# Kernel optimization log

Measured on AMD Instinct MI355X. Metric: run time of the kernel, lower is better.

Reference implementation:

```python
import jax, jax.numpy as jnp
import numpy as np
jax.config.update("jax_enable_x64", True)

T_OLD = 60000
T_NEW = 60000
NV = 30000
MAX_STEPS = 300
FB_CHUNK = 500  # T_OLD must be divisible by this

FACE_OPP = np.array([[1, 2, 3], [0, 2, 3], [0, 1, 3], [0, 1, 2]])
EDGES = [(0, 1), (0, 2), (0, 3), (1, 2), (1, 3), (2, 3)]


def setup_inputs() -> dict:
    key = jax.random.key(0)
    k1, k2, k3, k4, k5 = jax.random.split(key, 5)
    # distinct vertices per tet (sorted base + strictly increasing offsets)
    off = jnp.arange(4, dtype=jnp.int64)
    new_indices = jnp.sort(jax.random.randint(k1, (T_NEW, 4), 0, NV - 4, dtype=jnp.int64), axis=1) + off
    old_indices = jnp.sort(jax.random.randint(k2, (T_OLD, 4), 0, NV - 4, dtype=jnp.int64), axis=1) + off
    return {
        "new_indices": new_indices,
        "old_indices": old_indices,
        "old_cc": jax.random.normal(k3, (T_OLD, 3), dtype=jnp.float32),
        "new_cc": jax.random.normal(k4, (T_NEW, 3), dtype=jnp.float32),
        "vertex_positions": jax.random.uniform(k5, (NV, 3), dtype=jnp.float32),
    }


def _min_edge_length(verts, indices):
    p = verts[indices]  # (T,4,3)
    el = jnp.stack([jnp.linalg.norm(p[:, a] - p[:, b], axis=-1) for a, b in EDGES])
    return el.min(axis=0)


def _forward(new_indices, old_indices, old_cc, new_cc, vertex_positions):
    T_new = new_indices.shape[0]
    T_old = old_indices.shape[0]
    Vn = vertex_positions.shape[0]

    # --- 1. unchanged-tet detection via sorted-vertex int64 keys ---
    key4 = lambda s: ((s[:, 0] * Vn + s[:, 1]) * Vn + s[:, 2]) * Vn + s[:, 3]
    ok = key4(jnp.sort(old_indices, axis=1))
    nk = key4(jnp.sort(new_indices, axis=1))
    order = jnp.argsort(ok)
    sk = ok[order]
    pos = jnp.searchsorted(sk, nk, side='right') - 1
    posc = jnp.clip(pos, 0, T_old - 1)
    matched = jnp.where((pos >= 0) & (sk[posc] == nk), order[posc], -1)
    is_matched = matched >= 0
    matched_safe = jnp.maximum(matched, 0)

    # --- 2. face adjacency of old mesh (sorted face keys, adjacent-equal pairing) ---
    fi = jnp.sort(old_indices[:, FACE_OPP], axis=2)          # (T_old,4,3)
    fk = (fi[..., 0] * Vn + fi[..., 1]) * Vn + fi[..., 2]    # (T_old,4)
    all_keys = fk.T.reshape(-1)                              # f-major like the numpy concat
    all_tets = jnp.tile(jnp.arange(T_old), 4)
    all_locals = jnp.repeat(jnp.arange(4), T_old)
    o2 = jnp.argsort(all_keys)
    sk2, st, sl = all_keys[o2], all_tets[o2], all_locals[o2]
    same = sk2[:-1] == sk2[1:]
    neighbors = jnp.full((T_old, 4), -1, dtype=jnp.int64)
    neighbors = neighbors.at[jnp.where(same, st[:-1], T_old), sl[:-1]].set(st[1:], mode='drop')
    neighbors = neighbors.at[jnp.where(same, st[1:], T_old), sl[1:]].set(st[:-1], mode='drop')

    # --- 3. per-old-tet inverse edge matrix; degenerate tets get no neighbors ---
    verts = jax.lax.stop_gradient(vertex_positions).astype(jnp.float32)
    p = verts[old_indices]                                   # (T_old,4,3)
    v0 = p[:, 0]
    Tm = jnp.stack([p[:, 1] - v0, p[:, 2] - v0, p[:, 3] - v0], axis=-1)
    degen = jnp.abs(jnp.linalg.det(Tm)) < 1e-10
    Tinv = jnp.linalg.inv(jnp.where(degen[:, None, None], jnp.eye(3, dtype=Tm.dtype), Tm))
    neighbors = jnp.where(degen[:, None], -1, neighbors)

    prio = jnp.full((Vn,), -1, dtype=jnp.int64)
    ar = jnp.arange(T_old)
    for vi in range(4):
        prio = prio.at[old_indices[:, vi]].max(vi * T_old + ar)
    v2t = jnp.where(prio >= 0, prio % T_old, 0)

    # --- 5. barycentric walk (masked, all float inputs stop-gradiented; int outputs) ---
    cent = jax.lax.stop_gradient(verts[new_indices].mean(axis=1))  # (T_new,3)
    seed = v2t[new_indices[:, 0]]
    n_walk = jnp.sum(~is_matched)
    thr = jnp.maximum(jnp.int64(100), n_walk // 1000)

    def cond(state):
        step, cur, rem, act = state
        return (step < MAX_STEPS) & (jnp.sum(act) >= thr)

    def body(state):
        step, cur, rem, act = state
        rel = cent - v0[cur]
        bary = jnp.einsum('nij,nj->ni', Tinv[cur], rel)
        all_b = jnp.concatenate([(1.0 - bary.sum(axis=1))[:, None], bary], axis=1)
        conv = act & (all_b.min(axis=1) >= -1e-4)
        rem = jnp.where(conv, cur, rem)
        act = act & ~conv
        nb = neighbors[cur, jnp.argmin(all_b, axis=1)]
        at_bd = act & (nb < 0)
        rem = jnp.where(at_bd, cur, rem)
        act = act & ~at_bd
        cur = jnp.where(act, nb, cur)
        return (step + 1, cur, rem, act)

    _, cur, rem, act = jax.lax.while_loop(cond, body, (jnp.int64(0), seed, seed, ~is_matched))
    rem = jnp.where(act, cur, rem)

    # --- 6. nearest-centroid fallback for unfinished walks (gated, chunked) ---
    old_cents = jax.lax.stop_gradient(verts[old_indices].mean(axis=1))

    def fallback(_):
        p2 = (cent ** 2).sum(-1)
        c2 = (old_cents ** 2).sum(-1)
        def scan_body(carry, i):
            bd, bi = carry
            c = jax.lax.dynamic_slice(old_cents, (i * FB_CHUNK, 0), (FB_CHUNK, 3))
            cn = jax.lax.dynamic_slice(c2, (i * FB_CHUNK,), (FB_CHUNK,))
            d = p2[:, None] - 2.0 * (cent @ c.T) + cn[None, :]
            md = d.min(axis=1)
            mi = d.argmin(axis=1).astype(jnp.int64) + i * FB_CHUNK
            imp = md < bd
            return (jnp.where(imp, md, bd), jnp.where(imp, mi, bi)), None
        init = (jnp.full((T_new,), jnp.inf, dtype=jnp.float32), jnp.zeros((T_new,), dtype=jnp.int64))
        (bd, bi), _ = jax.lax.scan(scan_body, init, jnp.arange(T_old // FB_CHUNK))
        return bi

    fb = jax.lax.cond(jnp.sum(act) > 0, fallback, lambda _: jnp.zeros((T_new,), dtype=jnp.int64), None)
    rem = jnp.clip(jnp.where(act, fb, rem), 0, T_old - 1)
    remap = jnp.where(is_matched, matched_safe, rem)

    # --- 7. candidates: containing tet + 4 face neighbors ---
    face_nb = neighbors[remap]
    face_nb = jnp.where(face_nb >= 0, face_nb, remap[:, None])
    cands = jnp.concatenate([remap[:, None], face_nb], axis=1)            # (T_new,5)
    cands = jnp.where(is_matched[:, None], matched_safe[:, None], cands)

    # --- 8. overlap / circumcenter-distance weights ---
    cand_verts = old_indices[cands]                                       # (T_new,5,4)
    overlap = (cand_verts[:, :, :, None] == new_indices[:, None, None, :]).any(-1).sum(-1).astype(jnp.float32)
    cc_d2 = ((old_cc[cands] - new_cc[:, None, :]) ** 2).sum(-1)
    raw = jnp.exp(overlap * 2.0) / (cc_d2 + 1e-8)
    weights = raw / raw.sum(axis=1, keepdims=True)

    # --- 9. density scale: min-edge-length ratio ---
    old_el = _min_edge_length(vertex_positions, old_indices)[cands]
    new_el = _min_edge_length(vertex_positions, new_indices)
    density_scale = jnp.clip(old_el / jnp.maximum(new_el[:, None], 1e-8), 0.1, 10.0)

    return cands, weights, density_scale


_forward_jit = jax.jit(_forward)


def reference(new_indices, old_indices, old_cc, new_cc, vertex_positions):
    return _forward_jit(new_indices, old_indices, old_cc, new_cc, vertex_positions)
```

## Files before the change

### kernel.cpp

```cpp
#include <hip/hip_runtime.h>

#pragma clang fp contract(off)

#define TOLD 60000
#define TNEW 60000
#define NVERT 30000
#define MAXSTEPS 300
#define THSZ 131072
#define FHSZ 131072
#define EMPTY64 0xFFFFFFFFFFFFFFFFULL
#define NWGR 60
#define VRANGE 500
#define NSLICE 16
#define TSLICE (TOLD / NSLICE)

#define NB_SETUP 235
#define NB_PRIO  (NWGR * NSLICE)
#define NB_NEWG  235
#define NB_FACE  938
#define NB_FOLD  118
#define NB_MATCH 235
#define NB_FB    120
#define FBRANGE  (TNEW / NB_FB)

#define OFF_TKEYS    0u
#define OFF_FTAB     1048576u
#define OFF_NBR      2097152u
#define FF_BYTES     3057152u
#define OFF_CNT      3057152u
#define OFF_TVALS    3059200u
#define OFF_PPRIO    3583488u
#define OFF_PRIO     5503488u
#define OFF_IDXOLD   5623488u
#define OFF_SSTEP    6583488u
#define OFF_DEGEN    6823488u
#define OFF_MATCHED  7063488u
#define OFF_TV4      7303488u
#define OFF_COLD4    10183488u
#define OFF_CNEW4    11143488u
#define OFF_DM       12103488u

struct P {
  const unsigned int* rawNew;
  const unsigned int* rawOld;
  const float* occ;
  const float* ncc;
  const float* verts;
  float* out;
  unsigned long long* tkeys;
  unsigned long long* ftab;
  int* counters;
  int* tvals;
  int* idxOld;
  int* nbr;
  int* pprio;
  int* prio;
  int* sstep;
  int* degen;
  int* matched;
  float4* Tv4;
  float4* cold4;
  float4* cnew4;
  unsigned long long* dm;
  unsigned int dmMask;
};

__device__ __forceinline__ unsigned hash64(unsigned long long k){
  k ^= k >> 33; k *= 0xff51afd7ed558ccdULL;
  k ^= k >> 33; k *= 0xc4ceb9fe1a85ec53ULL;
  k ^= k >> 33;
  return (unsigned)k;
}
__device__ __forceinline__ void cswap(int& a, int& b){ if (a > b){ int t = a; a = b; b = t; } }

__device__ __forceinline__ int detect64(const unsigned int* raw){
  unsigned acc = 0;
  const uint4* r4 = (const uint4*)raw;
  #pragma unroll
  for (int k = 0; k < 32; ++k){ uint4 v = r4[k]; acc |= (v.y | v.w); }
  return acc == 0u;
}

__device__ __forceinline__ int4 load_tet4(const unsigned int* raw, int is64, int t){
  if (is64){
    uint4 a = ((const uint4*)raw)[t * 2 + 0];
    uint4 b = ((const uint4*)raw)[t * 2 + 1];
    return make_int4((int)a.x, (int)a.z, (int)b.x, (int)b.z);
  }
  uint4 a = ((const uint4*)raw)[t];
  return make_int4((int)a.x, (int)a.y, (int)a.z, (int)a.w);
}

__device__ __forceinline__ void face_insert(unsigned long long* ftab, int* nbr,
                                            unsigned long long fkey, int t, int l){
  unsigned long long mine = (fkey << 18) | (unsigned long long)(t * 4 + l);
  unsigned slot = hash64(fkey ^ 0x9e3779b97f4a7c15ULL) & (FHSZ - 1);
  while (true){
    unsigned long long prev = atomicCAS(&ftab[slot], EMPTY64, mine);
    if (prev == EMPTY64) return;
    if ((prev >> 18) == fkey){
      int oid = (int)(prev & 0x3FFFFULL);
      nbr[t * 4 + l] = oid >> 2;
      nbr[oid] = t;
      return;
    }
    slot = (slot + 1) & (FHSZ - 1);
  }
}

__device__ __forceinline__ float min_edge_r(
    float q0x, float q0y, float q0z, float q1x, float q1y, float q1z,
    float q2x, float q2y, float q2z, float q3x, float q3y, float q3z){
  float m = 3.402823466e+38f;
  float dx, dy, dz, d;
  dx = q0x - q1x; dy = q0y - q1y; dz = q0z - q1z; d = sqrtf((dx*dx + dy*dy) + dz*dz); m = fminf(m, d);
  dx = q0x - q2x; dy = q0y - q2y; dz = q0z - q2z; d = sqrtf((dx*dx + dy*dy) + dz*dz); m = fminf(m, d);
  dx = q0x - q3x; dy = q0y - q3y; dz = q0z - q3z; d = sqrtf((dx*dx + dy*dy) + dz*dz); m = fminf(m, d);
  dx = q1x - q2x; dy = q1y - q2y; dz = q1z - q2z; d = sqrtf((dx*dx + dy*dy) + dz*dz); m = fminf(m, d);
  dx = q1x - q3x; dy = q1y - q3y; dz = q1z - q3z; d = sqrtf((dx*dx + dy*dy) + dz*dz); m = fminf(m, d);
  dx = q2x - q3x; dy = q2y - q3y; dz = q2z - q3z; d = sqrtf((dx*dx + dy*dy) + dz*dz); m = fminf(m, d);
  return m;
}

__global__ __launch_bounds__(256) void k_front(P p){
  __shared__ int sprio[VRANGE];
  int bb = blockIdx.x;
  if (bb < NB_SETUP){
    int t = bb * 256 + threadIdx.x;
    if (bb == 0){
      for (int j = threadIdx.x; j < 384; j += 256) p.counters[j] = 0;
    }
    if (t >= TOLD) return;
    int is64 = detect64(p.rawOld);
    int4 iv4 = load_tet4(p.rawOld, is64, t);
    int i0 = iv4.x, i1 = iv4.y, i2 = iv4.z, i3 = iv4.w;
    ((int4*)p.idxOld)[t] = iv4;

    {
      int s0 = i0, s1 = i1, s2 = i2, s3 = i3;
      cswap(s0, s1); cswap(s2, s3); cswap(s0, s2); cswap(s1, s3); cswap(s1, s2);
      unsigned long long key =
          (unsigned long long)((((long long)s0 * NVERT + s1) * NVERT + s2) * NVERT + s3);
      unsigned slot = hash64(key) & (THSZ - 1);
      while (true){
        unsigned long long prev = atomicCAS(&p.tkeys[slot], EMPTY64, key);
        if (prev == EMPTY64){ p.tvals[slot] = t; break; }
        if (prev == key){ atomicMax(&p.tvals[slot], t); break; }
        slot = (slot + 1) & (THSZ - 1);
      }
    }

    if (p.dmMask){
      const int FO[4][3] = {{1, 2, 3}, {0, 2, 3}, {0, 1, 3}, {0, 1, 2}};
      int iv[4] = {i0, i1, i2, i3};
      #pragma unroll
      for (int l = 0; l < 4; ++l){
        int a = iv[FO[l][0]], b = iv[FO[l][1]], c = iv[FO[l][2]];
        cswap(a, b); cswap(a, c); cswap(b, c);
        unsigned long long fk = (unsigned long long)(((long long)a * NVERT + b) * NVERT + c);
        p.dm[hash64(fk) & p.dmMask] = (fk << 18) | (unsigned long long)(t * 4 + l);
      }
    }

    float q0x = p.verts[i0 * 3 + 0], q0y = p.verts[i0 * 3 + 1], q0z = p.verts[i0 * 3 + 2];
    float q1x = p.verts[i1 * 3 + 0], q1y = p.verts[i1 * 3 + 1], q1z = p.verts[i1 * 3 + 2];
    float q2x = p.verts[i2 * 3 + 0], q2y = p.verts[i2 * 3 + 1], q2z = p.verts[i2 * 3 + 2];
    float q3x = p.verts[i3 * 3 + 0], q3y = p.verts[i3 * 3 + 1], q3z = p.verts[i3 * 3 + 2];
    float e1x = q1x - q0x, e1y = q1y - q0y, e1z = q1z - q0z;
    float e2x = q2x - q0x, e2y = q2y - q0y, e2z = q2z - q0z;
    float e3x = q3x - q0x, e3y = q3y - q0y, e3z = q3z - q0z;
    float c23x = e2y * e3z - e2z * e3y;
    float c23y = e2z * e3x - e2x * e3z;
    float c23z = e2x * e3y - e2y * e3x;
    float det = e1x * c23x + e1y * c23y + e1z * c23z;
    int dg = (fabsf(det) < 1e-10f) ? 1 : 0;
    p.degen[t] = dg;
    float4 r0, r1, r2;
    if (dg){
      r0 = make_float4(1.f, 0.f, 0.f, q0x);
      r1 = make_float4(0.f, 1.f, 0.f, q0y);
      r2 = make_float4(0.f, 0.f, 1.f, q0z);
    } else {
      float inv = 1.0f / det;
      float c31x = e3y * e1z - e3z * e1y;
      float c31y = e3z * e1x - e3x * e1z;
      float c31z = e3x * e1y - e3y * e1x;
      float c12x = e1y * e2z - e1z * e2y;
      float c12y = e1z * e2x - e1x * e2z;
      float c12z = e1x * e2y - e1y * e2x;
      r0 = make_float4(c23x * inv, c23y * inv, c23z * inv, q0x);
      r1 = make_float4(c31x * inv, c31y * inv, c31z * inv, q0y);
      r2 = make_float4(c12x * inv, c12y * inv, c12z * inv, q0z);
    }
    p.Tv4[t * 3 + 0] = r0;
    p.Tv4[t * 3 + 1] = r1;
    p.Tv4[t * 3 + 2] = r2;
    float el = min_edge_r(q0x, q0y, q0z, q1x, q1y, q1z, q2x, q2y, q2z, q3x, q3y, q3z);
    p.cold4[t] = make_float4((((q0x + q1x) + q2x) + q3x) * 0.25f,
                             (((q0y + q1y) + q2y) + q3y) * 0.25f,
                             (((q0z + q1z) + q2z) + q3z) * 0.25f, el);
  } else if (bb < NB_SETUP + NB_PRIO){
    int rb = bb - NB_SETUP;
    int range = rb / NSLICE;
    int slice = rb % NSLICE;
    int base = range * VRANGE;
    for (int j = threadIdx.x; j < VRANGE; j += 256) sprio[j] = -1;
    __syncthreads();
    int is64 = detect64(p.rawOld);
    int t0 = slice * TSLICE;
    for (int t = t0 + threadIdx.x; t < t0 + TSLICE; t += 256){
      int4 iv = load_tet4(p.rawOld, is64, t);
      int v;
      v = iv.x - base; if ((unsigned)v < VRANGE) atomicMax(&sprio[v], 0 * TOLD + t);
      v = iv.y - base; if ((unsigned)v < VRANGE) atomicMax(&sprio[v], 1 * TOLD + t);
      v = iv.z - base; if ((unsigned)v < VRANGE) atomicMax(&sprio[v], 2 * TOLD + t);
      v = iv.w - base; if ((unsigned)v < VRANGE) atomicMax(&sprio[v], 3 * TOLD + t);
    }
    __syncthreads();
    for (int j = threadIdx.x; j < VRANGE; j += 256)
      p.pprio[slice * NVERT + base + j] = sprio[j];
  } else {
    int n = (bb - NB_SETUP - NB_PRIO) * 256 + threadIdx.x;
    if (n >= TNEW) return;
    int is64 = detect64(p.rawNew);
    int4 ni = load_tet4(p.rawNew, is64, n);
    float q0x = p.verts[ni.x * 3 + 0], q0y = p.verts[ni.x * 3 + 1], q0z = p.verts[ni.x * 3 + 2];
    float q1x = p.verts[ni.y * 3 + 0], q1y = p.verts[ni.y * 3 + 1], q1z = p.verts[ni.y * 3 + 2];
    float q2x = p.verts[ni.z * 3 + 0], q2y = p.verts[ni.z * 3 + 1], q2z = p.verts[ni.z * 3 + 2];
    float q3x = p.verts[ni.w * 3 + 0], q3y = p.verts[ni.w * 3 + 1], q3z = p.verts[ni.w * 3 + 2];
    float el = min_edge_r(q0x, q0y, q0z, q1x, q1y, q1z, q2x, q2y, q2z, q3x, q3y, q3z);
    p.cnew4[n] = make_float4((((q0x + q1x) + q2x) + q3x) * 0.25f,
                             (((q0y + q1y) + q2y) + q3y) * 0.25f,
                             (((q0z + q1z) + q2z) + q3z) * 0.25f, el);
  }
}

__global__ __launch_bounds__(256) void k_mid(P p){
  int bb = blockIdx.x;
  if (bb < NB_FACE){
    int i = bb * 256 + threadIdx.x;
    if (i >= TOLD * 4) return;
    int t = i >> 2, l = i & 3;
    int4 iv4 = ((const int4*)p.idxOld)[t];
    int iv[4] = {iv4.x, iv4.y, iv4.z, iv4.w};
    const int FO[4][3] = {{1, 2, 3}, {0, 2, 3}, {0, 1, 3}, {0, 1, 2}};
    int a = iv[FO[l][0]], b = iv[FO[l][1]], c = iv[FO[l][2]];
    cswap(a, b); cswap(a, c); cswap(b, c);
    unsigned long long fk = (unsigned long long)(((long long)a * NVERT + b) * NVERT + c);
    if (p.dmMask){
      unsigned long long mine = (fk << 18) | (unsigned long long)i;
      unsigned long long got = p.dm[hash64(fk) & p.dmMask];
      if (got == mine) return;
      if ((got >> 18) == fk){
        int wid = (int)(got & 0x3FFFFULL);
        p.nbr[i] = wid >> 2;
        p.nbr[wid] = t;
        return;
      }
    }
    face_insert(p.ftab, p.nbr, fk, t, l);
  } else if (bb < NB_FACE + NB_FOLD){
    int v = (bb - NB_FACE) * 256 + threadIdx.x;
    if (v >= NVERT) return;
    int pr = -1;
    #pragma unroll
    for (int s = 0; s < NSLICE; ++s) pr = max(pr, p.pprio[s * NVERT + v]);
    p.prio[v] = pr;
  } else {
    int n = (bb - NB_FACE - NB_FOLD) * 256 + threadIdx.x;
    if (n >= TNEW) return;
    int is64 = detect64(p.rawNew);
    int4 ni = load_tet4(p.rawNew, is64, n);
    int s0 = ni.x, s1 = ni.y, s2 = ni.z, s3 = ni.w;
    cswap(s0, s1); cswap(s2, s3); cswap(s0, s2); cswap(s1, s3); cswap(s1, s2);
    unsigned long long key =
        (unsigned long long)((((long long)s0 * NVERT + s1) * NVERT + s2) * NVERT + s3);
    int m = -1;
    unsigned slot = hash64(key) & (THSZ - 1);
    while (true){
      unsigned long long k = p.tkeys[slot];
      if (k == EMPTY64) break;
      if (k == key){ m = p.tvals[slot]; break; }
      slot = (slot + 1) & (THSZ - 1);
    }
    p.matched[n] = m;
  }
}

__device__ __forceinline__ void assemble_walker(const P& p, int n, int m, int remap){
  int cds[5];
  if (m >= 0){
    cds[0] = cds[1] = cds[2] = cds[3] = cds[4] = m;
  } else {
    cds[0] = remap;
    int dg = p.degen[remap];
    int4 nb4 = ((const int4*)p.nbr)[remap];
    int nbl[4] = {nb4.x, nb4.y, nb4.z, nb4.w};
    for (int l = 0; l < 4; ++l){
      int fb = dg ? -1 : nbl[l];
      cds[1 + l] = (fb >= 0) ? fb : remap;
    }
  }
  bool same = (cds[1] == cds[0]) & (cds[2] == cds[0]) &
              (cds[3] == cds[0]) & (cds[4] == cds[0]);
  int is64 = detect64(p.rawNew);
  int4 ni = load_tet4(p.rawNew, is64, n);
  float nc0 = p.ncc[n * 3 + 0], nc1 = p.ncc[n * 3 + 1], nc2 = p.ncc[n * 3 + 2];
  float nelv = fmaxf(p.cnew4[n].w, 1e-8f);
  if (same){
    int ct = cds[0];
    int4 cv = ((const int4*)p.idxOld)[ct];
    int ov = 0;
    ov += (cv.x == ni.x || cv.x == ni.y || cv.x == ni.z || cv.x == ni.w) ? 1 : 0;
    ov += (cv.y == ni.x || cv.y == ni.y || cv.y == ni.z || cv.y == ni.w) ? 1 : 0;
    ov += (cv.z == ni.x || cv.z == ni.y || cv.z == ni.z || cv.z == ni.w) ? 1 : 0;
    ov += (cv.w == ni.x || cv.w == ni.y || cv.w == ni.z || cv.w == ni.w) ? 1 : 0;
    float d0 = p.occ[ct * 3 + 0] - nc0;
    float d1 = p.occ[ct * 3 + 1] - nc1;
    float d2 = p.occ[ct * 3 + 2] - nc2;
    float ccd2 = (d0 * d0 + d1 * d1) + d2 * d2;
    float raw = expf((float)ov * 2.0f) / (ccd2 + 1e-8f);
    float rsum = 0.0f;
    rsum += raw; rsum += raw; rsum += raw; rsum += raw; rsum += raw;
    float wgt = raw / rsum;
    float ds = p.cold4[ct].w / nelv;
    ds = fminf(fmaxf(ds, 0.1f), 10.0f);
    float cf = (float)ct;
    for (int c = 0; c < 5; ++c){
      p.out[n * 5 + c] = cf;
      p.out[TNEW * 5 + n * 5 + c] = wgt;
      p.out[2 * TNEW * 5 + n * 5 + c] = ds;
    }
    return;
  }
  float raws[5]; float rsum = 0.0f;
  float oels[5];
  for (int c = 0; c < 5; ++c){
    int ct = cds[c];
    int4 cv = ((const int4*)p.idxOld)[ct];
    int ov = 0;
    ov += (cv.x == ni.x || cv.x == ni.y || cv.x == ni.z || cv.x == ni.w) ? 1 : 0;
    ov += (cv.y == ni.x || cv.y == ni.y || cv.y == ni.z || cv.y == ni.w) ? 1 : 0;
    ov += (cv.z == ni.x || cv.z == ni.y || cv.z == ni.z || cv.z == ni.w) ? 1 : 0;
    ov += (cv.w == ni.x || cv.w == ni.y || cv.w == ni.z || cv.w == ni.w) ? 1 : 0;
    float d0 = p.occ[ct * 3 + 0] - nc0;
    float d1 = p.occ[ct * 3 + 1] - nc1;
    float d2 = p.occ[ct * 3 + 2] - nc2;
    float ccd2 = (d0 * d0 + d1 * d1) + d2 * d2;
    float raw = expf((float)ov * 2.0f) / (ccd2 + 1e-8f);
    raws[c] = raw; rsum += raw;
    oels[c] = p.cold4[ct].w;
  }
  for (int c = 0; c < 5; ++c){
    p.out[n * 5 + c] = (float)cds[c];
    p.out[TNEW * 5 + n * 5 + c] = raws[c] / rsum;
    float ds = oels[c] / nelv;
    ds = fminf(fmaxf(ds, 0.1f), 10.0f);
    p.out[2 * TNEW * 5 + n * 5 + c] = ds;
  }
}

__global__ __launch_bounds__(256) void k_walkall(P p){
  __shared__ int s_hist[MAXSTEPS + 2];
  __shared__ int s_nw;
  for (int j = threadIdx.x; j < MAXSTEPS + 2; j += 256) s_hist[j] = 0;
  if (threadIdx.x == 0) s_nw = 0;
  __syncthreads();
  int n = blockIdx.x * blockDim.x + threadIdx.x;
  if (n < TNEW){
    int m = p.matched[n];
    if (m >= 0){
      assemble_walker(p, n, m, 0);
    } else {
      atomicAdd(&s_nw, 1);
      int is64 = detect64(p.rawNew);
      int i0 = is64 ? (int)((const long long*)p.rawNew)[n * 4] : ((const int*)p.rawNew)[n * 4];
      int pr = p.prio[i0];
      int c = (pr >= 0) ? (pr % TOLD) : 0;
      float4 cn = p.cnew4[n];
      int s = MAXSTEPS + 1;
      for (int k = 1; k <= MAXSTEPS; ++k){
        float4 r0 = p.Tv4[c * 3 + 0];
        float4 r1 = p.Tv4[c * 3 + 1];
        float4 r2 = p.Tv4[c * 3 + 2];
        float rx = cn.x - r0.w, ry = cn.y - r1.w, rz = cn.z - r2.w;
        float b0 = r0.x * rx + r0.y * ry + r0.z * rz;
        float b1 = r1.x * rx + r1.y * ry + r1.z * rz;
        float b2 = r2.x * rx + r2.y * ry + r2.z * rz;
        float a0 = 1.0f - (b0 + b1 + b2);
        float ab[4] = {a0, b0, b1, b2};
        int amin = 0; float mn = ab[0];
        for (int j = 1; j < 4; ++j){ if (ab[j] < mn){ mn = ab[j]; amin = j; } }
        if (mn >= -0.0001f){ s = k; break; }
        int nb = p.degen[c] ? -1 : p.nbr[c * 4 + amin];
        if (nb < 0){ s = k; break; }
        c = nb;
      }
      p.sstep[n] = s;
      atomicAdd(&s_hist[s], 1);
      assemble_walker(p, n, -1, c);
    }
  }
  __syncthreads();
  if (threadIdx.x == 0 && s_nw) atomicAdd(&p.counters[0], s_nw);
  for (int j = threadIdx.x; j < MAXSTEPS + 2; j += 256){
    int v = s_hist[j];
    if (v) atomicAdd(&p.counters[64 + j], v);
  }
}

__device__ __forceinline__ int compute_S(const int* counters){
  int nw = counters[0];
  int thr = max(100, nw / 1000);
  if (nw < thr) return 0;
  int cnt = nw;
  for (int k = 1; k <= MAXSTEPS; ++k){
    cnt -= counters[64 + k];
    if (cnt < thr) return k;
  }
  return MAXSTEPS;
}

__global__ __launch_bounds__(256) void k_tail(P p){
  __shared__ float sd[256];
  __shared__ int si[256];
  __shared__ int s_hits[256];
  __shared__ int s_nhits;
  __shared__ int s_S;
  if (threadIdx.x == 0) s_S = compute_S(p.counters);
  __syncthreads();
  int S = s_S;
  int base = blockIdx.x * FBRANGE;
  for (int chunk = base; chunk < base + FBRANGE; chunk += 256){
    if (threadIdx.x == 0) s_nhits = 0;
    __syncthreads();
    int n = chunk + threadIdx.x;
    if (n < base + FBRANGE && n < TNEW){
      if (p.matched[n] < 0 && p.sstep[n] > S)
        s_hits[atomicAdd(&s_nhits, 1)] = n;
    }
    __syncthreads();
    int nh = s_nhits;
    for (int h = 0; h < nh; ++h){
      int n2 = s_hits[h];
      float4 cn = p.cnew4[n2];
      float cx = cn.x, cy = cn.y, cz = cn.z;
      float p2 = (cx * cx + cy * cy) + cz * cz;
      float bd = 3.402823466e+38f; int bi = 0;
      for (int j = threadIdx.x; j < TOLD; j += 256){
        float4 oc = p.cold4[j];
        float dot = (cx * oc.x + cy * oc.y) + cz * oc.z;
        float c2 = (oc.x * oc.x + oc.y * oc.y) + oc.z * oc.z;
        float d = (p2 - 2.0f * dot) + c2;
        if (d < bd || (d == bd && j < bi)){ bd = d; bi = j; }
      }
      sd[threadIdx.x] = bd; si[threadIdx.x] = bi;
      __syncthreads();
      for (int s = 128; s > 0; s >>= 1){
        if ((int)threadIdx.x < s){
          float od = sd[threadIdx.x + s]; int oi = si[threadIdx.x + s];
          if (od < sd[threadIdx.x] || (od == sd[threadIdx.x] && oi < si[threadIdx.x])){
            sd[threadIdx.x] = od; si[threadIdx.x] = oi;
          }
        }
        __syncthreads();
      }
      if (threadIdx.x == 0){
        int r = si[0];
        if (r < 0) r = 0; if (r > TOLD - 1) r = TOLD - 1;
        assemble_walker(p, n2, -1, r);
      }
      __syncthreads();
    }
    __syncthreads();
  }
}

extern "C" void kernel_launch(void* const* d_in, const int* in_sizes, int n_in,
                              void* d_out, int out_size, void* d_ws, size_t ws_size,
                              hipStream_t stream) {
  char* w = (char*)d_ws;
  P p;
  p.rawNew = (const unsigned int*)d_in[0];
  p.rawOld = (const unsigned int*)d_in[1];
  p.occ    = (const float*)d_in[2];
  p.ncc    = (const float*)d_in[3];
  p.verts  = (const float*)d_in[4];
  p.out    = (float*)d_out;
  p.tkeys    = (unsigned long long*)(w + OFF_TKEYS);
  p.ftab     = (unsigned long long*)(w + OFF_FTAB);
  p.nbr      = (int*)(w + OFF_NBR);
  p.counters = (int*)(w + OFF_CNT);
  p.tvals    = (int*)(w + OFF_TVALS);
  p.pprio    = (int*)(w + OFF_PPRIO);
  p.prio     = (int*)(w + OFF_PRIO);
  p.idxOld   = (int*)(w + OFF_IDXOLD);
  p.sstep    = (int*)(w + OFF_SSTEP);
  p.degen    = (int*)(w + OFF_DEGEN);
  p.matched  = (int*)(w + OFF_MATCHED);
  p.Tv4      = (float4*)(w + OFF_TV4);
  p.cold4    = (float4*)(w + OFF_COLD4);
  p.cnew4    = (float4*)(w + OFF_CNEW4);
  p.dm       = (unsigned long long*)(w + OFF_DM);
  size_t avail = (ws_size > (size_t)OFF_DM) ? ws_size - (size_t)OFF_DM : 0;
  unsigned dmMask = 0;
  for (int bshift = 21; bshift >= 16; --bshift){
    if (avail >= ((size_t)8 << bshift)){ dmMask = (1u << bshift) - 1u; break; }
  }
  p.dmMask = dmMask;

  hipMemsetAsync(w, 0xFF, FF_BYTES, stream);
  hipLaunchKernelGGL(k_front,   dim3(NB_SETUP + NB_PRIO + NB_NEWG), dim3(256), 0, stream, p);
  hipLaunchKernelGGL(k_mid,     dim3(NB_FACE + NB_FOLD + NB_MATCH), dim3(256), 0, stream, p);
  hipLaunchKernelGGL(k_walkall, dim3((TNEW + 255) / 256), dim3(256), 0, stream, p);
  hipLaunchKernelGGL(k_tail,    dim3(NB_FB), dim3(256), 0, stream, p);
}
```

Before: 113.7 us.

## Replace CAS tet hash with direct-mapped table plus fallback, fuse match into walker

Tet-key deduplication now writes keys into a large direct-mapped table without atomics. Duplicate resolution and collisions are deferred to the face pass, where a CAS-based fallback table handles them. The workspace memset is replaced by init blocks inside the first kernel, and new-tet geometry and the match lookup move into the walker kernel, removing the separate matched array and an extra pass. Correctness depends on the non-atomic direct-map writes: the key write for a slot can race, and setting tval2 by plain store loses last-write-wins semantics when duplicate keys exist.

Result: faster. 109.5 us (-3.7%).

```diff
diff --git a/kernel.cpp b/kernel.cpp
--- a/kernel.cpp
+++ b/kernel.cpp
@@ -6,7 +6,8 @@
 #define TNEW 60000
 #define NVERT 30000
 #define MAXSTEPS 300
-#define THSZ 131072
+#define TKSZ 262144
+#define TFBSZ 131072
 #define FHSZ 131072
 #define EMPTY64 0xFFFFFFFFFFFFFFFFULL
 #define NWGR 60
@@ -16,29 +17,31 @@
 
 #define NB_SETUP 235
 #define NB_PRIO  (NWGR * NSLICE)
-#define NB_NEWG  235
+#define NB_INIT  187
 #define NB_FACE  938
 #define NB_FOLD  118
-#define NB_MATCH 235
+#define NB_WALK  235
 #define NB_FB    120
 #define FBRANGE  (TNEW / NB_FB)
 
-#define OFF_TKEYS    0u
-#define OFF_FTAB     1048576u
+#define OFF_FTAB     0u
+#define OFF_TFB      1048576u
 #define OFF_NBR      2097152u
 #define FF_BYTES     3057152u
+#define FF_UINT4     191072u
 #define OFF_CNT      3057152u
-#define OFF_TVALS    3059200u
+#define OFF_TFV      3059200u
 #define OFF_PPRIO    3583488u
 #define OFF_PRIO     5503488u
 #define OFF_IDXOLD   5623488u
 #define OFF_SSTEP    6583488u
 #define OFF_DEGEN    6823488u
-#define OFF_MATCHED  7063488u
-#define OFF_TV4      7303488u
-#define OFF_COLD4    10183488u
-#define OFF_CNEW4    11143488u
-#define OFF_DM       12103488u
+#define OFF_TV4      7063488u
+#define OFF_COLD4    9943488u
+#define OFF_CNEW4    10903488u
+#define OFF_TKEY2    11863488u
+#define OFF_TVAL2    13960640u
+#define OFF_DM       15009216u
 
 struct P {
   const unsigned int* rawNew;
@@ -47,17 +50,18 @@
   const float* ncc;
   const float* verts;
   float* out;
-  unsigned long long* tkeys;
+  unsigned long long* tkey2;
+  int* tval2;
+  unsigned long long* tfb;
+  int* tfv;
   unsigned long long* ftab;
   int* counters;
-  int* tvals;
   int* idxOld;
   int* nbr;
   int* pprio;
   int* prio;
   int* sstep;
   int* degen;
-  int* matched;
   float4* Tv4;
   float4* cold4;
   float4* cnew4;
@@ -126,10 +130,10 @@
   __shared__ int sprio[VRANGE];
   int bb = blockIdx.x;
   if (bb < NB_SETUP){
-    int t = bb * 256 + threadIdx.x;
     if (bb == 0){
       for (int j = threadIdx.x; j < 384; j += 256) p.counters[j] = 0;
     }
+    int t = bb * 256 + threadIdx.x;
     if (t >= TOLD) return;
     int is64 = detect64(p.rawOld);
     int4 iv4 = load_tet4(p.rawOld, is64, t);
@@ -141,13 +145,7 @@
       cswap(s0, s1); cswap(s2, s3); cswap(s0, s2); cswap(s1, s3); cswap(s1, s2);
       unsigned long long key =
           (unsigned long long)((((long long)s0 * NVERT + s1) * NVERT + s2) * NVERT + s3);
-      unsigned slot = hash64(key) & (THSZ - 1);
-      while (true){
-        unsigned long long prev = atomicCAS(&p.tkeys[slot], EMPTY64, key);
-        if (prev == EMPTY64){ p.tvals[slot] = t; break; }
-        if (prev == key){ atomicMax(&p.tvals[slot], t); break; }
-        slot = (slot + 1) & (THSZ - 1);
-      }
+      p.tkey2[hash64(key) & (TKSZ - 1)] = key;
     }
 
     if (p.dmMask){
@@ -220,18 +218,14 @@
     for (int j = threadIdx.x; j < VRANGE; j += 256)
       p.pprio[slice * NVERT + base + j] = sprio[j];
   } else {
-    int n = (bb - NB_SETUP - NB_PRIO) * 256 + threadIdx.x;
-    if (n >= TNEW) return;
-    int is64 = detect64(p.rawNew);
-    int4 ni = load_tet4(p.rawNew, is64, n);
-    float q0x = p.verts[ni.x * 3 + 0], q0y = p.verts[ni.x * 3 + 1], q0z = p.verts[ni.x * 3 + 2];
-    float q1x = p.verts[ni.y * 3 + 0], q1y = p.verts[ni.y * 3 + 1], q1z = p.verts[ni.y * 3 + 2];
-    float q2x = p.verts[ni.z * 3 + 0], q2y = p.verts[ni.z * 3 + 1], q2z = p.verts[ni.z * 3 + 2];
-    float q3x = p.verts[ni.w * 3 + 0], q3y = p.verts[ni.w * 3 + 1], q3z = p.verts[ni.w * 3 + 2];
-    float el = min_edge_r(q0x, q0y, q0z, q1x, q1y, q1z, q2x, q2y, q2z, q3x, q3y, q3z);
-    p.cnew4[n] = make_float4((((q0x + q1x) + q2x) + q3x) * 0.25f,
-                             (((q0y + q1y) + q2y) + q3y) * 0.25f,
-                             (((q0z + q1z) + q2z) + q3z) * 0.25f, el);
+    unsigned idx = (unsigned)(bb - NB_SETUP - NB_PRIO) * 1024u + threadIdx.x * 4u;
+    uint4 ff = make_uint4(~0u, ~0u, ~0u, ~0u);
+    uint4* base = (uint4*)p.ftab;
+    #pragma unroll
+    for (unsigned k = 0; k < 4; ++k){
+      unsigned id = idx + k;
+      if (id < FF_UINT4) base[id] = ff;
+    }
   }
 }
 
@@ -243,6 +237,26 @@
     int t = i >> 2, l = i & 3;
     int4 iv4 = ((const int4*)p.idxOld)[t];
     int iv[4] = {iv4.x, iv4.y, iv4.z, iv4.w};
+
+    if (l == 0){
+      int s0 = iv4.x, s1 = iv4.y, s2 = iv4.z, s3 = iv4.w;
+      cswap(s0, s1); cswap(s2, s3); cswap(s0, s2); cswap(s1, s3); cswap(s1, s2);
+      unsigned long long key =
+          (unsigned long long)((((long long)s0 * NVERT + s1) * NVERT + s2) * NVERT + s3);
+      unsigned slot = hash64(key) & (TKSZ - 1);
+      if (p.tkey2[slot] == key){
+        p.tval2[slot] = t;
+      } else {
+        unsigned fs = hash64(key ^ 0x517cc1b727220a95ULL) & (TFBSZ - 1);
+        while (true){
+          unsigned long long prev = atomicCAS(&p.tfb[fs], EMPTY64, key);
+          if (prev == EMPTY64){ p.tfv[fs] = t; break; }
+          if (prev == key){ atomicMax(&p.tfv[fs], t); break; }
+          fs = (fs + 1) & (TFBSZ - 1);
+        }
+      }
+    }
+
     const int FO[4][3] = {{1, 2, 3}, {0, 2, 3}, {0, 1, 3}, {0, 1, 2}};
     int a = iv[FO[l][0]], b = iv[FO[l][1]], c = iv[FO[l][2]];
     cswap(a, b); cswap(a, c); cswap(b, c);
@@ -259,35 +273,18 @@
       }
     }
     face_insert(p.ftab, p.nbr, fk, t, l);
-  } else if (bb < NB_FACE + NB_FOLD){
+  } else {
     int v = (bb - NB_FACE) * 256 + threadIdx.x;
     if (v >= NVERT) return;
     int pr = -1;
     #pragma unroll
     for (int s = 0; s < NSLICE; ++s) pr = max(pr, p.pprio[s * NVERT + v]);
     p.prio[v] = pr;
-  } else {
-    int n = (bb - NB_FACE - NB_FOLD) * 256 + threadIdx.x;
-    if (n >= TNEW) return;
-    int is64 = detect64(p.rawNew);
-    int4 ni = load_tet4(p.rawNew, is64, n);
-    int s0 = ni.x, s1 = ni.y, s2 = ni.z, s3 = ni.w;
-    cswap(s0, s1); cswap(s2, s3); cswap(s0, s2); cswap(s1, s3); cswap(s1, s2);
-    unsigned long long key =
-        (unsigned long long)((((long long)s0 * NVERT + s1) * NVERT + s2) * NVERT + s3);
-    int m = -1;
-    unsigned slot = hash64(key) & (THSZ - 1);
-    while (true){
-      unsigned long long k = p.tkeys[slot];
-      if (k == EMPTY64) break;
-      if (k == key){ m = p.tvals[slot]; break; }
-      slot = (slot + 1) & (THSZ - 1);
-    }
-    p.matched[n] = m;
-  }
-}
-
-__device__ __forceinline__ void assemble_walker(const P& p, int n, int m, int remap){
+  }
+}
+
+__device__ __forceinline__ void assemble_walker(const P& p, int n, int m, int remap,
+                                                int4 ni, float nelv){
   int cds[5];
   if (m >= 0){
     cds[0] = cds[1] = cds[2] = cds[3] = cds[4] = m;
@@ -303,10 +300,7 @@
   }
   bool same = (cds[1] == cds[0]) & (cds[2] == cds[0]) &
               (cds[3] == cds[0]) & (cds[4] == cds[0]);
-  int is64 = detect64(p.rawNew);
-  int4 ni = load_tet4(p.rawNew, is64, n);
   float nc0 = p.ncc[n * 3 + 0], nc1 = p.ncc[n * 3 + 1], nc2 = p.ncc[n * 3 + 2];
-  float nelv = fmaxf(p.cnew4[n].w, 1e-8f);
   if (same){
     int ct = cds[0];
     int4 cv = ((const int4*)p.idxOld)[ct];
@@ -368,16 +362,46 @@
   __syncthreads();
   int n = blockIdx.x * blockDim.x + threadIdx.x;
   if (n < TNEW){
-    int m = p.matched[n];
+    int is64 = detect64(p.rawNew);
+    int4 ni = load_tet4(p.rawNew, is64, n);
+
+    float q0x = p.verts[ni.x * 3 + 0], q0y = p.verts[ni.x * 3 + 1], q0z = p.verts[ni.x * 3 + 2];
+    float q1x = p.verts[ni.y * 3 + 0], q1y = p.verts[ni.y * 3 + 1], q1z = p.verts[ni.y * 3 + 2];
+    float q2x = p.verts[ni.z * 3 + 0], q2y = p.verts[ni.z * 3 + 1], q2z = p.verts[ni.z * 3 + 2];
+    float q3x = p.verts[ni.w * 3 + 0], q3y = p.verts[ni.w * 3 + 1], q3z = p.verts[ni.w * 3 + 2];
+    float el = min_edge_r(q0x, q0y, q0z, q1x, q1y, q1z, q2x, q2y, q2z, q3x, q3y, q3z);
+    float4 cn = make_float4((((q0x + q1x) + q2x) + q3x) * 0.25f,
+                            (((q0y + q1y) + q2y) + q3y) * 0.25f,
+                            (((q0z + q1z) + q2z) + q3z) * 0.25f, el);
+    p.cnew4[n] = cn;
+    float nelv = fmaxf(el, 1e-8f);
+
+    int m = -1;
+    {
+      int s0 = ni.x, s1 = ni.y, s2 = ni.z, s3 = ni.w;
+      cswap(s0, s1); cswap(s2, s3); cswap(s0, s2); cswap(s1, s3); cswap(s1, s2);
+      unsigned long long key =
+          (unsigned long long)((((long long)s0 * NVERT + s1) * NVERT + s2) * NVERT + s3);
+      unsigned slot = hash64(key) & (TKSZ - 1);
+      if (p.tkey2[slot] == key){
+        m = p.tval2[slot];
+      } else {
+        unsigned fs = hash64(key ^ 0x517cc1b727220a95ULL) & (TFBSZ - 1);
+        while (true){
+          unsigned long long k2 = p.tfb[fs];
+          if (k2 == EMPTY64) break;
+          if (k2 == key){ m = p.tfv[fs]; break; }
+          fs = (fs + 1) & (TFBSZ - 1);
+        }
+      }
+    }
     if (m >= 0){
-      assemble_walker(p, n, m, 0);
+      p.sstep[n] = 0;
+      assemble_walker(p, n, m, 0, ni, nelv);
     } else {
       atomicAdd(&s_nw, 1);
-      int is64 = detect64(p.rawNew);
-      int i0 = is64 ? (int)((const long long*)p.rawNew)[n * 4] : ((const int*)p.rawNew)[n * 4];
-      int pr = p.prio[i0];
+      int pr = p.prio[ni.x];
       int c = (pr >= 0) ? (pr % TOLD) : 0;
-      float4 cn = p.cnew4[n];
       int s = MAXSTEPS + 1;
       for (int k = 1; k <= MAXSTEPS; ++k){
         float4 r0 = p.Tv4[c * 3 + 0];
@@ -398,7 +422,7 @@
       }
       p.sstep[n] = s;
       atomicAdd(&s_hist[s], 1);
-      assemble_walker(p, n, -1, c);
+      assemble_walker(p, n, -1, c, ni, nelv);
     }
   }
   __syncthreads();
@@ -436,7 +460,7 @@
     __syncthreads();
     int n = chunk + threadIdx.x;
     if (n < base + FBRANGE && n < TNEW){
-      if (p.matched[n] < 0 && p.sstep[n] > S)
+      if (p.sstep[n] > S)
         s_hits[atomicAdd(&s_nhits, 1)] = n;
     }
     __syncthreads();
@@ -468,7 +492,10 @@
       if (threadIdx.x == 0){
         int r = si[0];
         if (r < 0) r = 0; if (r > TOLD - 1) r = TOLD - 1;
-        assemble_walker(p, n2, -1, r);
+        int is64 = detect64(p.rawNew);
+        int4 ni = load_tet4(p.rawNew, is64, n2);
+        float nelv = fmaxf(p.cnew4[n2].w, 1e-8f);
+        assemble_walker(p, n2, -1, r, ni, nelv);
       }
       __syncthreads();
     }
@@ -487,31 +514,31 @@
   p.ncc    = (const float*)d_in[3];
   p.verts  = (const float*)d_in[4];
   p.out    = (float*)d_out;
-  p.tkeys    = (unsigned long long*)(w + OFF_TKEYS);
   p.ftab     = (unsigned long long*)(w + OFF_FTAB);
+  p.tfb      = (unsigned long long*)(w + OFF_TFB);
   p.nbr      = (int*)(w + OFF_NBR);
   p.counters = (int*)(w + OFF_CNT);
-  p.tvals    = (int*)(w + OFF_TVALS);
+  p.tfv      = (int*)(w + OFF_TFV);
   p.pprio    = (int*)(w + OFF_PPRIO);
   p.prio     = (int*)(w + OFF_PRIO);
   p.idxOld   = (int*)(w + OFF_IDXOLD);
   p.sstep    = (int*)(w + OFF_SSTEP);
   p.degen    = (int*)(w + OFF_DEGEN);
-  p.matched  = (int*)(w + OFF_MATCHED);
   p.Tv4      = (float4*)(w + OFF_TV4);
   p.cold4    = (float4*)(w + OFF_COLD4);
   p.cnew4    = (float4*)(w + OFF_CNEW4);
+  p.tkey2    = (unsigned long long*)(w + OFF_TKEY2);
+  p.tval2    = (int*)(w + OFF_TVAL2);
   p.dm       = (unsigned long long*)(w + OFF_DM);
   size_t avail = (ws_size > (size_t)OFF_DM) ? ws_size - (size_t)OFF_DM : 0;
   unsigned dmMask = 0;
-  for (int bshift = 21; bshift >= 16; --bshift){
+  for (int bshift = 22; bshift >= 16; --bshift){
     if (avail >= ((size_t)8 << bshift)){ dmMask = (1u << bshift) - 1u; break; }
   }
   p.dmMask = dmMask;
 
-  hipMemsetAsync(w, 0xFF, FF_BYTES, stream);
-  hipLaunchKernelGGL(k_front,   dim3(NB_SETUP + NB_PRIO + NB_NEWG), dim3(256), 0, stream, p);
-  hipLaunchKernelGGL(k_mid,     dim3(NB_FACE + NB_FOLD + NB_MATCH), dim3(256), 0, stream, p);
-  hipLaunchKernelGGL(k_walkall, dim3((TNEW + 255) / 256), dim3(256), 0, stream, p);
+  hipLaunchKernelGGL(k_front,   dim3(NB_SETUP + NB_PRIO + NB_INIT), dim3(256), 0, stream, p);
+  hipLaunchKernelGGL(k_mid,     dim3(NB_FACE + NB_FOLD), dim3(256), 0, stream, p);
+  hipLaunchKernelGGL(k_walkall, dim3(NB_WALK), dim3(256), 0, stream, p);
   hipLaunchKernelGGL(k_tail,    dim3(NB_FB), dim3(256), 0, stream, p);
 }
```
